# Kernel tuning notes

Measured on AMD Instinct MI355X. Metric: run time of the kernel, lower is better.

Reference implementation:

```python
import jax, jax.numpy as jnp
import numpy as np

# dims (match init_kwargs)
L, D, H, K = 8, 384, 6, 64            # layers, hidden, rwkv heads, rwkv head dim
DI, MH, HD, DS, CK = 768, 12, 64, 64, 4  # mamba: d_inner, heads, head_dim, d_state, conv kernel
V, B, T = 32000, 1, 1024


def _rms(x, w, eps=1e-6):
    return w * x * jax.lax.rsqrt(jnp.mean(x * x, axis=-1, keepdims=True) + eps)


def _rwkv6(xn, Wr, Wk, Wv, Wg, Ww, w_bias, u, gn_w, gn_b, Wo):
    # RWKV6: data-dependent diagonal-decay linear attention
    Bb, Tt, Dd = xn.shape
    proj = lambda W: (xn @ W).reshape(Bb, Tt, H, K)
    r, k, v = proj(Wr), proj(Wk), proj(Wv)
    g = xn @ Wg                                        # [B,T,D]
    w = (xn @ Ww + w_bias).reshape(Bb, Tt, H, K)
    decay = jnp.exp(-jnp.exp(w))                       # in (0,1)

    def step(S, inp):                                  # S: [B,H,K,K] (key x value)
        r_t, k_t, v_t, d_t = inp                       # each [B,H,K]
        kv = k_t[..., :, None] * v_t[..., None, :]     # [B,H,K,K]
        o = jnp.einsum('bhk,bhkv->bhv', r_t, S + u[None, :, :, None] * kv)
        S = d_t[..., None] * S + kv
        return S, o

    tm = lambda a: jnp.moveaxis(a, 1, 0)               # time-major
    S0 = jnp.zeros((Bb, H, K, K), xn.dtype)
    _, o = jax.lax.scan(step, S0, (tm(r), tm(k), tm(v), tm(decay)))
    o = jnp.moveaxis(o, 0, 1)                          # [B,T,H,K]
    # per-head GroupNorm
    mu = jnp.mean(o, -1, keepdims=True)
    var = jnp.var(o, -1, keepdims=True)
    o = (o - mu) * jax.lax.rsqrt(var + 1e-5) * gn_w.reshape(H, K) + gn_b.reshape(H, K)
    o = o.reshape(Bb, Tt, Dd) * jax.nn.silu(g)
    return o @ Wo


def _mamba2(xn, W_in, conv_w, conv_b, dt_bias, A_log, Dp, mn_w, W_out):
    # Mamba2: selective scan with scalar A per head
    Bb, Tt, Dd = xn.shape
    zxbcdt = xn @ W_in                                 # [B,T, 2*DI + 2*DS + MH]
    z = zxbcdt[..., :DI]
    xBC = zxbcdt[..., DI:DI + DI + 2 * DS]
    dt = jax.nn.softplus(zxbcdt[..., -MH:] + dt_bias)  # [B,T,MH]
    # causal depthwise conv1d, kernel CK
    xp = jnp.pad(xBC, ((0, 0), (CK - 1, 0), (0, 0)))
    xBC = sum(xp[:, j:j + Tt, :] * conv_w[:, j] for j in range(CK)) + conv_b
    xBC = jax.nn.silu(xBC)
    xs = xBC[..., :DI].reshape(Bb, Tt, MH, HD)
    Bm = xBC[..., DI:DI + DS]                          # [B,T,DS]
    Cm = xBC[..., DI + DS:]                            # [B,T,DS]
    A = -jnp.exp(A_log)                                # [MH]

    def step(S, inp):                                  # S: [B,MH,HD,DS]
        x_t, B_t, C_t, dt_t = inp                      # [B,MH,HD],[B,DS],[B,DS],[B,MH]
        dA = jnp.exp(dt_t * A)                         # [B,MH]
        S = dA[..., None, None] * S + (dt_t[..., None] * x_t)[..., None] * B_t[:, None, None, :]
        y = jnp.einsum('bhps,bs->bhp', S, C_t) + Dp[None, :, None] * x_t
        return S, y

    tm = lambda a: jnp.moveaxis(a, 1, 0)
    S0 = jnp.zeros((Bb, MH, HD, DS), xn.dtype)
    _, y = jax.lax.scan(step, S0, (tm(xs), tm(Bm), tm(Cm), tm(dt)))
    y = jnp.moveaxis(y, 0, 1).reshape(Bb, Tt, DI)
    y = _rms(y * jax.nn.silu(z), mn_w)                 # gated RMSNorm
    return y @ W_out


def _forward(x, embed, ln_w, Wr, Wk, Wv, Wg, Ww, w_bias, u, gn_w, gn_b, Wo,
             W_in, conv_w, conv_b, dt_bias, A_log, Dp, mn_w, W_out,
             gw, gb, ffn_ln_w, ffn_w1, ffn_w2, ln_out_w):
    h = jnp.take(embed, x, axis=0)                     # [B,T,D]
    for i in range(L):
        xn = _rms(h, ln_w[i])
        o_r = _rwkv6(xn, Wr[i], Wk[i], Wv[i], Wg[i], Ww[i], w_bias[i], u[i], gn_w[i], gn_b[i], Wo[i])
        o_m = _mamba2(xn, W_in[i], conv_w[i], conv_b[i], dt_bias[i], A_log[i], Dp[i], mn_w[i], W_out[i])
        gate = jax.nn.sigmoid(jnp.concatenate([o_r, o_m], -1) @ gw[i] + gb[i])  # [B,T,1]
        h = h + gate * o_r + (1.0 - gate) * o_m
        hn = _rms(h, ffn_ln_w[i])
        h = h + jax.nn.gelu(hn @ ffn_w1[i], approximate=False) @ ffn_w2[i]
    h = _rms(h, ln_out_w)
    return h @ embed.T                                 # tied head -> [B,T,V]


def setup_inputs() -> dict:
    key = jax.random.key(0)
    ks = iter(jax.random.split(key, 32))
    n = lambda shape, s=0.02: jax.random.normal(next(ks), shape, jnp.float32) * s
    d = {}
    d['x'] = jax.random.randint(next(ks), (B, T), 0, V)
    d['embed'] = n((V, D))
    d['ln_w'] = jnp.ones((L, D), jnp.float32)
    d['Wr'] = n((L, D, D)); d['Wk'] = n((L, D, D)); d['Wv'] = n((L, D, D))
    d['Wg'] = n((L, D, D)); d['Ww'] = n((L, D, D))
    d['w_bias'] = n((L, D), 0.5)
    d['u'] = n((L, H, K), 0.5)
    d['gn_w'] = jnp.ones((L, D), jnp.float32)
    d['gn_b'] = jnp.zeros((L, D), jnp.float32)
    d['Wo'] = n((L, D, D))
    d['W_in'] = n((L, D, 2 * DI + 2 * DS + MH))
    d['conv_w'] = n((L, DI + 2 * DS, CK), 0.2)
    d['conv_b'] = jnp.zeros((L, DI + 2 * DS), jnp.float32)
    d['dt_bias'] = jax.random.uniform(next(ks), (L, MH), jnp.float32, -4.0, -1.0)
    d['A_log'] = jnp.log(jax.random.uniform(next(ks), (L, MH), jnp.float32, 1.0, 16.0))
    d['Dp'] = jnp.ones((L, MH), jnp.float32)
    d['mn_w'] = jnp.ones((L, DI), jnp.float32)
    d['W_out'] = n((L, DI, D))
    d['gw'] = n((L, 2 * D, 1), 0.01)
    d['gb'] = jnp.full((L, 1), float(np.log(0.3 / 0.7)), jnp.float32)
    d['ffn_ln_w'] = jnp.ones((L, D), jnp.float32)
    d['ffn_w1'] = n((L, D, 4 * D))
    d['ffn_w2'] = n((L, 4 * D, D))
    d['ln_out_w'] = jnp.ones((D,), jnp.float32)
    return d


def reference(x, embed, ln_w, Wr, Wk, Wv, Wg, Ww, w_bias, u, gn_w, gn_b, Wo,
              W_in, conv_w, conv_b, dt_bias, A_log, Dp, mn_w, W_out,
              gw, gb, ffn_ln_w, ffn_w1, ffn_w2, ln_out_w):
    return _forward(x, embed, ln_w, Wr, Wk, Wv, Wg, Ww, w_bias, u, gn_w, gn_b, Wo,
                    W_in, conv_w, conv_b, dt_bias, A_log, Dp, mn_w, W_out,
                    gw, gb, ffn_ln_w, ffn_w1, ffn_w2, ln_out_w)
```

## Files before the change

kernel.cpp:

```cpp
#include <hip/hip_runtime.h>
#include <math.h>

#define TT 1024
#define DD 384
#define NH 6
#define DI 768
#define MH 12
#define DS 64
#define NL 8
#define XDIM 1676
#define CONVC 896
#define NV 32000
#define PZS 3712
#define G_OFF 1152
#define W_OFF 1536
#define Z_OFF 1920
#define XBC_OFF 2688
#define DT_OFF 3584
#define CHK 32
#define NCH 32

typedef __attribute__((ext_vector_type(8))) short short8;
typedef __attribute__((ext_vector_type(4))) float f32x4;

__device__ __forceinline__ float siluf(float x) { return x / (1.f + expf(-x)); }
__device__ __forceinline__ float sigmoidf_(float x) { return 1.f / (1.f + expf(-x)); }
__device__ __forceinline__ float geluf(float x) {
  return 0.5f * x * (1.f + erff(x * 0.70710678118654752440f));
}
__device__ __forceinline__ unsigned short f2b(float x) {
  union { float f; unsigned int u; } v; v.f = x;
  unsigned int r = v.u + 0x7fffu + ((v.u >> 16) & 1u);
  return (unsigned short)(r >> 16);
}

#define GLDS(gp, lp) __builtin_amdgcn_global_load_lds( \
    (const __attribute__((address_space(1))) void*)(gp), \
    (__attribute__((address_space(3))) void*)(lp), 16, 0, 0)

template<int EPI>
__global__ __launch_bounds__(256) void gemm_bf16(
    const unsigned short* __restrict__ A, const unsigned short* __restrict__ Bt,
    float* __restrict__ C, unsigned short* __restrict__ Cb, int N, int K, int ldC)
{
  __shared__ unsigned short As[4096];
  __shared__ unsigned short Bs[4096];
  int tid = threadIdx.x;
  int wid = tid >> 6, lane = tid & 63;
  int m0 = blockIdx.y * 64, n0 = blockIdx.x * 64;
  int wr = wid >> 1, wc = wid & 1;
  int r0 = tid >> 3, ch = tid & 7;
  int scs = (ch ^ (r0 & 7)) * 8;
  const unsigned short* ga = A  + (size_t)(m0 + r0) * K + scs;
  const unsigned short* gb = Bt + (size_t)(n0 + r0) * K + scs;
  unsigned short* la = As + wid * 512;
  unsigned short* lb = Bs + wid * 512;
  int fr = lane & 15, fc = lane >> 4;
  f32x4 zz = {0.f, 0.f, 0.f, 0.f};
  f32x4 acc[2][2];
  acc[0][0] = zz; acc[0][1] = zz; acc[1][0] = zz; acc[1][1] = zz;

  int kper = K / (int)gridDim.z;
  int ks = blockIdx.z * kper, ke = ks + kper;
  size_t row32 = (size_t)32 * K;
  for (int k0 = ks; k0 < ke; k0 += 64) {
    GLDS(ga + k0, la);
    GLDS(ga + k0 + row32, la + 2048);
    GLDS(gb + k0, lb);
    GLDS(gb + k0 + row32, lb + 2048);
    __syncthreads();
#pragma unroll
    for (int kh = 0; kh < 2; ++kh) {
      short8 af[2], bf[2];
#pragma unroll
      for (int mg = 0; mg < 2; ++mg) {
        int ar = wr * 32 + mg * 16 + fr;
        af[mg] = *reinterpret_cast<const short8*>(&As[ar * 64 + (((kh * 4 + fc) ^ (ar & 7)) * 8)]);
      }
#pragma unroll
      for (int ng = 0; ng < 2; ++ng) {
        int br = wc * 32 + ng * 16 + fr;
        bf[ng] = *reinterpret_cast<const short8*>(&Bs[br * 64 + (((kh * 4 + fc) ^ (br & 7)) * 8)]);
      }
#pragma unroll
      for (int mg = 0; mg < 2; ++mg)
#pragma unroll
        for (int ng = 0; ng < 2; ++ng)
          acc[mg][ng] = __builtin_amdgcn_mfma_f32_16x16x32_bf16(af[mg], bf[ng], acc[mg][ng], 0, 0, 0);
    }
    __syncthreads();
  }
#pragma unroll
  for (int mg = 0; mg < 2; ++mg)
#pragma unroll
    for (int ng = 0; ng < 2; ++ng) {
      int col = n0 + wc * 32 + ng * 16 + fr;
      if (col < N) {
#pragma unroll
        for (int j = 0; j < 4; ++j) {
          int row = m0 + wr * 32 + mg * 16 + fc * 4 + j;
          if (EPI == 1)      Cb[(size_t)row * ldC + col] = f2b(geluf(acc[mg][ng][j]));
          else if (EPI == 3) atomicAdd(&C[(size_t)row * ldC + col], acc[mg][ng][j]);
          else               C[(size_t)row * ldC + col]  = acc[mg][ng][j];
        }
      }
    }
}

__global__ __launch_bounds__(256) void gemm_dual(
    const unsigned short* __restrict__ A0, const unsigned short* __restrict__ B0t,
    float* __restrict__ C0, int K0, int ld0, int nx0, int nb0,
    const unsigned short* __restrict__ A1, const unsigned short* __restrict__ B1t,
    float* __restrict__ C1, int K1, int ld1, int nx1)
{
  __shared__ unsigned short As[4096];
  __shared__ unsigned short Bs[4096];
  int b = blockIdx.x;
  const unsigned short *A, *Bt; float* C; int K, ldC, bx, by;
  if (b < nb0) { A = A0; Bt = B0t; C = C0; K = K0; ldC = ld0; bx = b % nx0; by = b / nx0; }
  else { b -= nb0; A = A1; Bt = B1t; C = C1; K = K1; ldC = ld1; bx = b % nx1; by = b / nx1; }
  int tid = threadIdx.x;
  int wid = tid >> 6, lane = tid & 63;
  int m0 = by * 64, n0 = bx * 64;
  int wr = wid >> 1, wc = wid & 1;
  int r0 = tid >> 3, ch = tid & 7;
  int scs = (ch ^ (r0 & 7)) * 8;
  const unsigned short* ga = A  + (size_t)(m0 + r0) * K + scs;
  const unsigned short* gb = Bt + (size_t)(n0 + r0) * K + scs;
  unsigned short* la = As + wid * 512;
  unsigned short* lb = Bs + wid * 512;
  int fr = lane & 15, fc = lane >> 4;
  f32x4 zz = {0.f, 0.f, 0.f, 0.f};
  f32x4 acc[2][2];
  acc[0][0] = zz; acc[0][1] = zz; acc[1][0] = zz; acc[1][1] = zz;
  size_t row32 = (size_t)32 * K;
  for (int k0 = 0; k0 < K; k0 += 64) {
    GLDS(ga + k0, la);
    GLDS(ga + k0 + row32, la + 2048);
    GLDS(gb + k0, lb);
    GLDS(gb + k0 + row32, lb + 2048);
    __syncthreads();
#pragma unroll
    for (int kh = 0; kh < 2; ++kh) {
      short8 af[2], bf[2];
#pragma unroll
      for (int mg = 0; mg < 2; ++mg) {
        int ar = wr * 32 + mg * 16 + fr;
        af[mg] = *reinterpret_cast<const short8*>(&As[ar * 64 + (((kh * 4 + fc) ^ (ar & 7)) * 8)]);
      }
#pragma unroll
      for (int ng = 0; ng < 2; ++ng) {
        int br = wc * 32 + ng * 16 + fr;
        bf[ng] = *reinterpret_cast<const short8*>(&Bs[br * 64 + (((kh * 4 + fc) ^ (br & 7)) * 8)]);
      }
#pragma unroll
      for (int mg = 0; mg < 2; ++mg)
#pragma unroll
        for (int ng = 0; ng < 2; ++ng)
          acc[mg][ng] = __builtin_amdgcn_mfma_f32_16x16x32_bf16(af[mg], bf[ng], acc[mg][ng], 0, 0, 0);
    }
    __syncthreads();
  }
#pragma unroll
  for (int mg = 0; mg < 2; ++mg)
#pragma unroll
    for (int ng = 0; ng < 2; ++ng) {
      int col = n0 + wc * 32 + ng * 16 + fr;
#pragma unroll
      for (int j = 0; j < 4; ++j) {
        int row = m0 + wr * 32 + mg * 16 + fc * 4 + j;
        C[(size_t)row * ldC + col] = acc[mg][ng][j];
      }
    }
}

__global__ __launch_bounds__(256) void gemm128(
    const unsigned short* __restrict__ A, const unsigned short* __restrict__ Bt,
    float* __restrict__ C, int N, int K, int ldC)
{
  __shared__ unsigned short As[8192];
  __shared__ unsigned short Bs[8192];
  int tid = threadIdx.x;
  int wid = tid >> 6, lane = tid & 63;
  int m0 = blockIdx.y * 128, n0 = blockIdx.x * 128;
  int wr = wid >> 1, wc = wid & 1;
  int r0 = tid >> 3, ch = tid & 7;
  int scs = (ch ^ (r0 & 7)) * 8;
  const unsigned short* ga = A  + (size_t)(m0 + r0) * K + scs;
  const unsigned short* gb = Bt + (size_t)(n0 + r0) * K + scs;
  int fr = lane & 15, fc = lane >> 4;
  f32x4 zz = {0.f, 0.f, 0.f, 0.f};
  f32x4 acc[4][4];
#pragma unroll
  for (int i = 0; i < 4; i++)
#pragma unroll
    for (int j = 0; j < 4; j++) acc[i][j] = zz;

  size_t row32 = (size_t)32 * K;
  for (int k0 = 0; k0 < K; k0 += 64) {
#pragma unroll
    for (int i = 0; i < 4; ++i) {
      GLDS(ga + k0 + i * row32, As + i * 2048 + wid * 512);
      GLDS(gb + k0 + i * row32, Bs + i * 2048 + wid * 512);
    }
    __syncthreads();
#pragma unroll
    for (int kh = 0; kh < 2; ++kh) {
      short8 af[4], bf[4];
#pragma unroll
      for (int mg = 0; mg < 4; ++mg) {
        int ar = wr * 64 + mg * 16 + fr;
        af[mg] = *reinterpret_cast<const short8*>(&As[ar * 64 + (((kh * 4 + fc) ^ (ar & 7)) * 8)]);
      }
#pragma unroll
      for (int ng = 0; ng < 4; ++ng) {
        int br = wc * 64 + ng * 16 + fr;
        bf[ng] = *reinterpret_cast<const short8*>(&Bs[br * 64 + (((kh * 4 + fc) ^ (br & 7)) * 8)]);
      }
#pragma unroll
      for (int mg = 0; mg < 4; ++mg)
#pragma unroll
        for (int ng = 0; ng < 4; ++ng)
          acc[mg][ng] = __builtin_amdgcn_mfma_f32_16x16x32_bf16(af[mg], bf[ng], acc[mg][ng], 0, 0, 0);
    }
    __syncthreads();
  }
#pragma unroll
  for (int mg = 0; mg < 4; ++mg)
#pragma unroll
    for (int ng = 0; ng < 4; ++ng) {
      int col = n0 + wc * 64 + ng * 16 + fr;
      if (col < N) {
#pragma unroll
        for (int j = 0; j < 4; ++j) {
          int row = m0 + wr * 64 + mg * 16 + fc * 4 + j;
          C[(size_t)row * ldC + col] = acc[mg][ng][j];
        }
      }
    }
}

struct TCJob { const float* src; unsigned short* dst; int K, N, Npad, nx; size_t sStr, dStr; int tend; };
struct TC10 { TCJob j[10]; };

__global__ __launch_bounds__(256) void transconv_all(TC10 P)
{
  __shared__ float tile[32][33];
  int bid = blockIdx.x;
  int q = 0;
  while (bid >= P.j[q].tend) ++q;
  int tstart = (q == 0) ? 0 : P.j[q - 1].tend;
  TCJob jb = P.j[q];
  int local = bid - tstart;
  int bx = local % jb.nx, by = local / jb.nx;
  const float* src = jb.src + (size_t)blockIdx.y * jb.sStr;
  unsigned short* dst = jb.dst + (size_t)blockIdx.y * jb.dStr;
  int k0 = by * 32, n0 = bx * 32;
  int tx = threadIdx.x & 31, ty = threadIdx.x >> 5;
  for (int i = ty; i < 32; i += 8) {
    int k = k0 + i, n = n0 + tx;
    tile[i][tx] = (k < jb.K && n < jb.N) ? src[(size_t)k * jb.N + n] : 0.f;
  }
  __syncthreads();
  for (int i = ty; i < 32; i += 8) {
    int n = n0 + i, k = k0 + tx;
    if (n < jb.Npad && k < jb.K) dst[(size_t)n * jb.K + k] = f2b(tile[tx][i]);
  }
}

__global__ void conv_b16_kernel(const float* __restrict__ src, unsigned short* __restrict__ dst, int n)
{
  int idx = blockIdx.x * 256 + threadIdx.x;
  if (idx < n) dst[idx] = f2b(src[idx]);
}

__global__ void embed_kernel(const int* __restrict__ x, const float* __restrict__ embed,
                             float* __restrict__ h)
{
  int idx = blockIdx.x * 256 + threadIdx.x;
  if (idx < TT * DD) {
    int t = idx / DD, d = idx % DD;
    h[idx] = embed[(size_t)x[t] * DD + d];
  }
}

__global__ __launch_bounds__(256) void rms_kernel(const float* __restrict__ in,
                                                  const float* __restrict__ w,
                                                  unsigned short* __restrict__ out)
{
  int row = blockIdx.x * 4 + (threadIdx.x >> 6);
  int lane = threadIdx.x & 63;
  const float* r = in + (size_t)row * DD;
  float v[6]; float ss = 0.f;
#pragma unroll
  for (int j = 0; j < 6; ++j) { v[j] = r[lane + j * 64]; ss = fmaf(v[j], v[j], ss); }
#pragma unroll
  for (int s = 1; s < 64; s <<= 1) ss += __shfl_xor(ss, s);
  float scale = rsqrtf(ss * (1.f / DD) + 1e-6f);
#pragma unroll
  for (int j = 0; j < 6; ++j)
    out[(size_t)row * DD + lane + j * 64] = f2b(w[lane + j * 64] * v[j] * scale);
}

__global__ __launch_bounds__(256) void scanA_kernel(
    const float* __restrict__ PZ, const float* __restrict__ u, const float* __restrict__ wbias,
    float* __restrict__ so, float* __restrict__ rPb,
    float* __restrict__ MstR, float* __restrict__ DcR,
    const float* __restrict__ cw, const float* __restrict__ cbia,
    const float* __restrict__ dtbias,
    const float* __restrict__ Alog, const float* __restrict__ Dpw,
    float* __restrict__ yb, float* __restrict__ Ccb,
    float* __restrict__ MstM, float* __restrict__ DcM)
{
  __shared__ float smem[2 * 256 + 64];
  int b = blockIdx.x, tid = threadIdx.x;
  if (b < 192) {
    int h = b >> 5, c = b & 31;
    float* sbuf = smem; float* us = smem + 512;
    if (tid < 64) us[tid] = u[h * 64 + tid];
    int wv = tid >> 6, l = tid & 63;
    int vv = wv * 16 + (l & 15);
    int kc = l >> 4;
    int arr = tid >> 6, idx = tid & 63;
    int off = (arr == 0) ? 0 : (arr == 1) ? 384 : (arr == 2) ? W_OFF : 768;
    float wb = (arr == 2) ? wbias[h * 64 + idx] : 0.f;
    size_t base = (size_t)h * 64 + idx + off;
    int t0 = c * CHK;
    float S[16], Pc[16];
#pragma unroll
    for (int i = 0; i < 16; i++) { S[i] = 0.f; Pc[i] = 1.f; }
    float reg = PZ[(size_t)t0 * PZS + base];
    bool st = (wv == 0) && ((l & 15) == 0);
    for (int t = 0; t < CHK; ++t) {
      int tt = t0 + t;
      float* cb = sbuf + (t & 1) * 256;
      cb[arr * 64 + idx] = (arr == 2) ? expf(-expf(reg + wb)) : reg;
      if (t + 1 < CHK) reg = PZ[(size_t)(tt + 1) * PZS + base];
      __syncthreads();
      float vt = cb[192 + vv];
      float acc = 0.f;
      float rp[16];
#pragma unroll
      for (int i = 0; i < 16; ++i) {
        int kk = kc * 16 + i;
        float rv = cb[kk], kv = cb[64 + kk], dv = cb[128 + kk];
        rp[i] = rv * Pc[i];
        float kvv = kv * vt;
        acc = fmaf(rv, fmaf(us[kk], kvv, S[i]), acc);
        S[i] = fmaf(dv, S[i], kvv);
        Pc[i] *= dv;
      }
      acc += __shfl_xor(acc, 16);
      acc += __shfl_xor(acc, 32);
      if (l < 16) so[(size_t)tt * DD + h * 64 + vv] = acc;
      if (st) {
        float4* dst = (float4*)&rPb[(size_t)tt * DD + h * 64 + kc * 16];
        dst[0] = make_float4(rp[0], rp[1], rp[2], rp[3]);
        dst[1] = make_float4(rp[4], rp[5], rp[6], rp[7]);
        dst[2] = make_float4(rp[8], rp[9], rp[10], rp[11]);
        dst[3] = make_float4(rp[12], rp[13], rp[14], rp[15]);
      }
    }
    float* ms = MstR + (size_t)(h * NCH + c) * 4096;
    float4* msv = (float4*)&ms[vv * 64 + kc * 16];
    msv[0] = make_float4(S[0], S[1], S[2], S[3]);
    msv[1] = make_float4(S[4], S[5], S[6], S[7]);
    msv[2] = make_float4(S[8], S[9], S[10], S[11]);
    msv[3] = make_float4(S[12], S[13], S[14], S[15]);
    if (st) {
      float4* dd_ = (float4*)&DcR[(h * NCH + c) * 64 + kc * 16];
      dd_[0] = make_float4(Pc[0], Pc[1], Pc[2], Pc[3]);
      dd_[1] = make_float4(Pc[4], Pc[5], Pc[6], Pc[7]);
      dd_[2] = make_float4(Pc[8], Pc[9], Pc[10], Pc[11]);
      dd_[3] = make_float4(Pc[12], Pc[13], Pc[14], Pc[15]);
    }
  } else {
    int bb = b - 192;
    int hh = bb >> 5, c = bb & 31;
    float* sbuf = smem;
    int wv = tid >> 6, l = tid & 63;
    int p = wv * 16 + (l & 15);
    int sc = l >> 4;
    int arr = tid >> 6, idx = tid & 63;
    float A = -expf(Alog[hh]);
    float Dph = Dpw[hh];
    float dtbh = dtbias[hh];
    int t0 = c * CHK;
    float cw0 = 0.f, cw1 = 0.f, cw2 = 0.f, cw3 = 0.f, cbv = 0.f;
    float xw0 = 0.f, xw1 = 0.f, xw2 = 0.f, cur = 0.f;
    const float* xcol = nullptr;
    float reg = 0.f;
    if (arr < 3) {
      int chn = (arr == 0) ? (hh * 64 + idx) : (arr == 1) ? (DI + idx) : (DI + DS + idx);
      cw0 = cw[chn * 4 + 0]; cw1 = cw[chn * 4 + 1]; cw2 = cw[chn * 4 + 2]; cw3 = cw[chn * 4 + 3];
      cbv = cbia[chn];
      xcol = PZ + XBC_OFF + chn;
      xw0 = (t0 >= 3) ? xcol[(size_t)(t0 - 3) * PZS] : 0.f;
      xw1 = (t0 >= 2) ? xcol[(size_t)(t0 - 2) * PZS] : 0.f;
      xw2 = (t0 >= 1) ? xcol[(size_t)(t0 - 1) * PZS] : 0.f;
      cur = xcol[(size_t)t0 * PZS];
    } else {
      reg = PZ[(size_t)t0 * PZS + DT_OFF + hh];
    }
    float S[16]; float cdA = 1.f;
#pragma unroll
    for (int i = 0; i < 16; i++) S[i] = 0.f;
    bool st = (wv == 0) && ((l & 15) == 0);
    for (int t = 0; t < CHK; ++t) {
      int tt = t0 + t;
      float* cb = sbuf + (t & 1) * 256;
      if (arr < 3) {
        float cvv = fmaf(cw3, cur, fmaf(cw2, xw2, fmaf(cw1, xw1, fmaf(cw0, xw0, cbv))));
        cb[arr * 64 + idx] = siluf(cvv);
        float nx = (t + 1 < CHK) ? xcol[(size_t)(tt + 1) * PZS] : 0.f;
        xw0 = xw1; xw1 = xw2; xw2 = cur; cur = nx;
      } else {
        if (idx == 0) {
          float v = reg + dtbh;
          cb[192] = (v > 20.f) ? v : log1pf(expf(v));
        }
        if (t + 1 < CHK) reg = PZ[(size_t)(tt + 1) * PZS + DT_OFF + hh];
      }
      __syncthreads();
      float dt_ = cb[192];
      float dA = expf(dt_ * A);
      cdA *= dA;
      float xp = cb[p];
      float dtx = dt_ * xp;
      float acc = 0.f;
#pragma unroll
      for (int i = 0; i < 16; ++i) {
        int s = sc * 16 + i;
        S[i] = fmaf(dA, S[i], dtx * cb[64 + s]);
        acc = fmaf(S[i], cb[128 + s], acc);
      }
      acc += __shfl_xor(acc, 16);
      acc += __shfl_xor(acc, 32);
      if (l < 16) yb[(size_t)tt * DI + hh * 64 + p] = fmaf(Dph, xp, acc);
      if (st) {
        float4* dst = (float4*)&Ccb[(size_t)tt * DI + hh * 64 + sc * 16];
#pragma unroll
        for (int j4 = 0; j4 < 4; ++j4)
          dst[j4] = make_float4(cdA * cb[128 + sc * 16 + j4 * 4 + 0],
                                cdA * cb[128 + sc * 16 + j4 * 4 + 1],
                                cdA * cb[128 + sc * 16 + j4 * 4 + 2],
                                cdA * cb[128 + sc * 16 + j4 * 4 + 3]);
      }
    }
    float* ms = MstM + (size_t)(hh * NCH + c) * 4096;
    float4* msv = (float4*)&ms[p * 64 + sc * 16];
    msv[0] = make_float4(S[0], S[1], S[2], S[3]);
    msv[1] = make_float4(S[4], S[5], S[6], S[7]);
    msv[2] = make_float4(S[8], S[9], S[10], S[11]);
    msv[3] = make_float4(S[12], S[13], S[14], S[15]);
    if (tid == 0) DcM[hh * NCH + c] = cdA;
  }
}

__global__ __launch_bounds__(256) void corr_kernel(
    const float* __restrict__ MstR, const float* __restrict__ DcR,
    const float* __restrict__ rPb, const float* __restrict__ so,
    const float* __restrict__ MstM, const float* __restrict__ DcM,
    const float* __restrict__ Ccb, float* __restrict__ yb,
    const float* __restrict__ PZ, const float* __restrict__ gnw, const float* __restrict__ gnb,
    unsigned short* __restrict__ gob)
{
  __shared__ float S0l[64 * 68];
  __shared__ float Rl[CHK * 68];
  int b = blockIdx.x, tid = threadIdx.x;
  const float* rg; int ostride, obase, t0;
  bool rwkv = (b < 192);
  int h, cidx;
  if (rwkv) {
    h = b >> 5; cidx = b & 31;
    rg = rPb; obase = h * 64; ostride = DD;
  } else {
    int bb = b - 192; h = bb >> 5; cidx = bb & 31;
    rg = Ccb; obase = h * 64; ostride = DI;
  }
  t0 = cidx * CHK;
  float Sreg[16];
#pragma unroll
  for (int it = 0; it < 16; ++it) Sreg[it] = 0.f;
  if (rwkv) {
    int kk = tid & 63;
    for (int cp = 0; cp < cidx; ++cp) {
      float d = DcR[(h * NCH + cp) * 64 + kk];
      const float* mb = MstR + (size_t)(h * NCH + cp) * 4096;
#pragma unroll
      for (int it = 0; it < 16; ++it)
        Sreg[it] = fmaf(d, Sreg[it], mb[tid + 256 * it]);
    }
  } else {
    for (int cp = 0; cp < cidx; ++cp) {
      float d = DcM[h * NCH + cp];
      const float* mb = MstM + (size_t)(h * NCH + cp) * 4096;
#pragma unroll
      for (int it = 0; it < 16; ++it)
        Sreg[it] = fmaf(d, Sreg[it], mb[tid + 256 * it]);
    }
  }
#pragma unroll
  for (int it = 0; it < 16; ++it) {
    int gi = tid + 256 * it;
    S0l[(gi & 63) * 68 + (gi >> 6)] = Sreg[it];
  }
  {
    int t = tid >> 3, q = (tid & 7) * 8;
    const float4* src = (const float4*)&rg[(size_t)(t0 + t) * ostride + obase + q];
    float4* dst = (float4*)&Rl[t * 68 + q];
    dst[0] = src[0]; dst[1] = src[1];
  }
  __syncthreads();
  int t = tid >> 3, q = (tid & 7) * 8;
  float acc[8];
#pragma unroll
  for (int j = 0; j < 8; j++) acc[j] = 0.f;
  for (int k = 0; k < 64; ++k) {
    float rv = Rl[t * 68 + k];
    const float4* sp = (const float4*)&S0l[k * 68 + q];
    float4 s0 = sp[0], s1 = sp[1];
    acc[0] = fmaf(rv, s0.x, acc[0]);
    acc[1] = fmaf(rv, s0.y, acc[1]);
    acc[2] = fmaf(rv, s0.z, acc[2]);
    acc[3] = fmaf(rv, s0.w, acc[3]);
    acc[4] = fmaf(rv, s1.x, acc[4]);
    acc[5] = fmaf(rv, s1.y, acc[5]);
    acc[6] = fmaf(rv, s1.z, acc[6]);
    acc[7] = fmaf(rv, s1.w, acc[7]);
  }
  if (!rwkv) {
    float4* op = (float4*)&yb[(size_t)(t0 + t) * DI + obase + q];
    float4 c0 = op[0], c1 = op[1];
    c0.x += acc[0]; c0.y += acc[1]; c0.z += acc[2]; c0.w += acc[3];
    c1.x += acc[4]; c1.y += acc[5]; c1.z += acc[6]; c1.w += acc[7];
    op[0] = c0; op[1] = c1;
  } else {
    float ov[8];
    const float4* sp = (const float4*)&so[(size_t)(t0 + t) * DD + obase + q];
    float4 s0 = sp[0], s1 = sp[1];
    ov[0] = s0.x + acc[0]; ov[1] = s0.y + acc[1]; ov[2] = s0.z + acc[2]; ov[3] = s0.w + acc[3];
    ov[4] = s1.x + acc[4]; ov[5] = s1.y + acc[5]; ov[6] = s1.z + acc[6]; ov[7] = s1.w + acc[7];
    float m_ = 0.f;
#pragma unroll
    for (int j = 0; j < 8; j++) m_ += ov[j];
    m_ += __shfl_xor(m_, 1); m_ += __shfl_xor(m_, 2); m_ += __shfl_xor(m_, 4);
    float mu = m_ * (1.f / 64.f);
    float vv = 0.f;
#pragma unroll
    for (int j = 0; j < 8; j++) { float d = ov[j] - mu; vv = fmaf(d, d, vv); }
    vv += __shfl_xor(vv, 1); vv += __shfl_xor(vv, 2); vv += __shfl_xor(vv, 4);
    float rstd = rsqrtf(vv * (1.f / 64.f) + 1e-5f);
#pragma unroll
    for (int j = 0; j < 8; j++) {
      int d = obase + q + j;
      float gv = PZ[(size_t)(t0 + t) * PZS + G_OFF + d];
      float o = fmaf((ov[j] - mu) * rstd, gnw[d], gnb[d]) * siluf(gv);
      gob[(size_t)(t0 + t) * DD + d] = f2b(o);
    }
  }
}

__global__ __launch_bounds__(256) void mamba_norm_kernel(const float* __restrict__ yb,
    const float* __restrict__ PZ, const float* __restrict__ mnw, unsigned short* __restrict__ out)
{
  int row = blockIdx.x * 4 + (threadIdx.x >> 6);
  int lane = threadIdx.x & 63;
  float v[12]; float ss = 0.f;
#pragma unroll
  for (int j = 0; j < 12; ++j) {
    int c = lane + j * 64;
    float z = PZ[(size_t)row * PZS + Z_OFF + c];
    float t = yb[(size_t)row * DI + c] * siluf(z);
    v[j] = t; ss = fmaf(t, t, ss);
  }
#pragma unroll
  for (int s = 1; s < 64; s <<= 1) ss += __shfl_xor(ss, s);
  float scale = rsqrtf(ss * (1.f / DI) + 1e-6f);
#pragma unroll
  for (int j = 0; j < 12; ++j) {
    int c = lane + j * 64;
    out[(size_t)row * DI + c] = f2b(v[j] * scale * mnw[c]);
  }
}

__global__ __launch_bounds__(256) void gate_rms_kernel(const float* __restrict__ orb,
    const float* __restrict__ omb, const float* __restrict__ gw,
    const float* __restrict__ gb, const float* __restrict__ flnw,
    float* __restrict__ h, unsigned short* __restrict__ xnb)
{
  int row = blockIdx.x * 4 + (threadIdx.x >> 6);
  int lane = threadIdx.x & 63;
  float a[6], bq[6]; float ss = 0.f;
#pragma unroll
  for (int j = 0; j < 6; ++j) {
    int c = lane + j * 64;
    a[j] = orb[(size_t)row * DD + c]; bq[j] = omb[(size_t)row * DD + c];
    ss += a[j] * gw[c] + bq[j] * gw[DD + c];
  }
#pragma unroll
  for (int s = 1; s < 64; s <<= 1) ss += __shfl_xor(ss, s);
  float gate = sigmoidf_(ss + gb[0]);
  float hn[6]; float ss2 = 0.f;
#pragma unroll
  for (int j = 0; j < 6; ++j) {
    int c = lane + j * 64;
    size_t ix = (size_t)row * DD + c;
    hn[j] = h[ix] + gate * a[j] + (1.f - gate) * bq[j];
    h[ix] = hn[j];
    ss2 = fmaf(hn[j], hn[j], ss2);
  }
#pragma unroll
  for (int s = 1; s < 64; s <<= 1) ss2 += __shfl_xor(ss2, s);
  float scale = rsqrtf(ss2 * (1.f / DD) + 1e-6f);
#pragma unroll
  for (int j = 0; j < 6; ++j) {
    int c = lane + j * 64;
    xnb[(size_t)row * DD + c] = f2b(flnw[c] * hn[j] * scale);
  }
}

extern "C" void kernel_launch(void* const* d_in, const int* in_sizes, int n_in,
                              void* d_out, int out_size, void* d_ws, size_t ws_size,
                              hipStream_t stream)
{
  const int*   x        = (const int*)  d_in[0];
  const float* embed    = (const float*)d_in[1];
  const float* ln_w     = (const float*)d_in[2];
  const float* Wr       = (const float*)d_in[3];
  const float* Wk       = (const float*)d_in[4];
  const float* Wv       = (const float*)d_in[5];
  const float* Wg       = (const float*)d_in[6];
  const float* Ww       = (const float*)d_in[7];
  const float* w_bias   = (const float*)d_in[8];
  const float* u        = (const float*)d_in[9];
  const float* gn_w     = (const float*)d_in[10];
  const float* gn_b     = (const float*)d_in[11];
  const float* Wo       = (const float*)d_in[12];
  const float* W_in     = (const float*)d_in[13];
  const float* conv_w   = (const float*)d_in[14];
  const float* conv_b   = (const float*)d_in[15];
  const float* dt_bias  = (const float*)d_in[16];
  const float* A_log    = (const float*)d_in[17];
  const float* Dp       = (const float*)d_in[18];
  const float* mn_w     = (const float*)d_in[19];
  const float* W_out    = (const float*)d_in[20];
  const float* gw       = (const float*)d_in[21];
  const float* gb       = (const float*)d_in[22];
  const float* ffn_ln_w = (const float*)d_in[23];
  const float* ffn_w1   = (const float*)d_in[24];
  const float* ffn_w2   = (const float*)d_in[25];
  const float* ln_out_w = (const float*)d_in[26];

  char* base = (char*)d_ws;
  size_t off = 0;
  auto alloc = [&](size_t bytes) { off = (off + 255) & ~(size_t)255; void* p = base + off; off += bytes; return p; };

  float* h    = (float*)alloc((size_t)TT * DD * 4);
  float* PZ   = (float*)alloc((size_t)TT * PZS * 4);
  float* yb   = (float*)alloc((size_t)TT * DI * 4);
  float* so   = (float*)alloc((size_t)TT * DD * 4);
  float* orb  = (float*)alloc((size_t)TT * DD * 4);
  float* omb  = (float*)alloc((size_t)TT * DD * 4);
  float* rPb  = (float*)alloc((size_t)TT * DD * 4);
  float* Ccb  = (float*)alloc((size_t)TT * DI * 4);
  float* MstR = (float*)alloc((size_t)NH * NCH * 4096 * 4);
  float* DcR  = (float*)alloc((size_t)NH * NCH * 64 * 4);
  float* MstM = (float*)alloc((size_t)MH * NCH * 4096 * 4);
  float* DcM  = (float*)alloc((size_t)MH * NCH * 4);
  unsigned short* xnb = (unsigned short*)alloc((size_t)TT * DD * 2);
  unsigned short* gob = (unsigned short*)alloc((size_t)TT * DD * 2);
  unsigned short* ynb = (unsigned short*)alloc((size_t)TT * DI * 2);
  unsigned short* fhb = (unsigned short*)alloc((size_t)TT * 1536 * 2);
  unsigned short* WallT = (unsigned short*)alloc((size_t)NL * PZS * 384 * 2);
  unsigned short* WoT   = (unsigned short*)alloc((size_t)NL * 384 * 384 * 2);
  unsigned short* WoutT = (unsigned short*)alloc((size_t)NL * 384 * 768 * 2);
  unsigned short* F1T   = (unsigned short*)alloc((size_t)NL * 1536 * 384 * 2);
  unsigned short* F2T   = (unsigned short*)alloc((size_t)NL * 384 * 1536 * 2);
  unsigned short* embB  = (unsigned short*)alloc((size_t)NV * DD * 2);
  (void)ws_size; (void)in_sizes; (void)n_in; (void)out_size;

  dim3 blk(256);
  int gTD = (TT * DD + 255) / 256;

  TC10 tc;
  int te = 0;
  auto setjob = [&](int q, const float* src, unsigned short* dst, int K, int N, int Npad,
                    int nx, int ny, size_t sStr, size_t dStr) {
    te += nx * ny;
    tc.j[q] = TCJob{src, dst, K, N, Npad, nx, sStr, dStr, te};
  };
  setjob(0, Wr, WallT + (size_t)0 * 384 * 384, 384, 384, 384, 12, 12, (size_t)384 * 384, (size_t)PZS * 384);
  setjob(1, Wk, WallT + (size_t)1 * 384 * 384, 384, 384, 384, 12, 12, (size_t)384 * 384, (size_t)PZS * 384);
  setjob(2, Wv, WallT + (size_t)2 * 384 * 384, 384, 384, 384, 12, 12, (size_t)384 * 384, (size_t)PZS * 384);
  setjob(3, Wg, WallT + (size_t)3 * 384 * 384, 384, 384, 384, 12, 12, (size_t)384 * 384, (size_t)PZS * 384);
  setjob(4, Ww, WallT + (size_t)4 * 384 * 384, 384, 384, 384, 12, 12, (size_t)384 * 384, (size_t)PZS * 384);
  setjob(5, W_in, WallT + (size_t)1920 * 384, 384, XDIM, 1792, 56, 12, (size_t)384 * XDIM, (size_t)PZS * 384);
  setjob(6, Wo, WoT, 384, 384, 384, 12, 12, (size_t)384 * 384, (size_t)384 * 384);
  setjob(7, W_out, WoutT, 768, 384, 384, 12, 24, (size_t)768 * 384, (size_t)384 * 768);
  setjob(8, ffn_w1, F1T, 384, 1536, 1536, 48, 12, (size_t)384 * 1536, (size_t)1536 * 384);
  setjob(9, ffn_w2, F2T, 1536, 384, 384, 12, 48, (size_t)1536 * 384, (size_t)384 * 1536);
  transconv_all<<<dim3(te, 8), blk, 0, stream>>>(tc);
  conv_b16_kernel<<<(NV * DD + 255) / 256, blk, 0, stream>>>(embed, embB, NV * DD);
  embed_kernel<<<gTD, blk, 0, stream>>>(x, embed, h);

  for (int i = 0; i < NL; ++i) {
    rms_kernel<<<256, blk, 0, stream>>>(h, ln_w + (size_t)i * DD, xnb);

    gemm_bf16<0><<<dim3(58, 16), blk, 0, stream>>>(
        xnb, WallT + (size_t)i * PZS * 384, PZ, nullptr, PZS, 384, PZS);

    scanA_kernel<<<576, blk, 0, stream>>>(PZ, u + (size_t)i * NH * 64, w_bias + (size_t)i * DD,
                                          so, rPb, MstR, DcR,
                                          conv_w + (size_t)i * CONVC * 4, conv_b + (size_t)i * CONVC,
                                          dt_bias + (size_t)i * MH,
                                          A_log + (size_t)i * MH, Dp + (size_t)i * MH,
                                          yb, Ccb, MstM, DcM);
    corr_kernel<<<576, blk, 0, stream>>>(MstR, DcR, rPb, so, MstM, DcM, Ccb, yb,
                                         PZ, gn_w + (size_t)i * DD, gn_b + (size_t)i * DD, gob);

    mamba_norm_kernel<<<256, blk, 0, stream>>>(yb, PZ, mn_w + (size_t)i * DI, ynb);

    gemm_dual<<<192, blk, 0, stream>>>(
        gob, WoT + (size_t)i * 384 * 384, orb, 384, DD, 6, 96,
        ynb, WoutT + (size_t)i * 384 * 768, omb, 768, DD, 6);

    gate_rms_kernel<<<256, blk, 0, stream>>>(orb, omb, gw + (size_t)i * 2 * DD, gb + i,
                                             ffn_ln_w + (size_t)i * DD, h, xnb);

    gemm_bf16<1><<<dim3(24, 16), blk, 0, stream>>>(
        xnb, F1T + (size_t)i * 1536 * 384, nullptr, fhb, 1536, 384, 1536);
    gemm_bf16<3><<<dim3(6, 16, 4), blk, 0, stream>>>(
        fhb, F2T + (size_t)i * 384 * 1536, h, nullptr, DD, 1536, DD);
  }

  rms_kernel<<<256, blk, 0, stream>>>(h, ln_out_w, xnb);
  gemm128<<<dim3(250, 8), blk, 0, stream>>>(
      xnb, embB, (float*)d_out, NV, 384, NV);
}
```

Baseline: 983.0 us.

## Remap LM-head GEMM tiles per XCD and stage stores through LDS

The final vocabulary GEMM now uses a 1D grid whose block index is remapped so that consecutive blocks on each XCD share the same embedding column tiles, which is meant to improve L2 reuse of the B operand. The epilogue stages each warp's accumulator fragment in shared memory and writes full rows with float4 stores, giving coalesced writes of the large fp32 logits output. The col<N guard is dropped, which holds only because 32000 is a multiple of 128. The staging adds extra syncthreads per tile.

```diff
diff --git a/kernel.cpp b/kernel.cpp
--- a/kernel.cpp
+++ b/kernel.cpp
@@ -178,11 +178,15 @@
     const unsigned short* __restrict__ A, const unsigned short* __restrict__ Bt,
     float* __restrict__ C, int N, int K, int ldC)
 {
-  __shared__ unsigned short As[8192];
-  __shared__ unsigned short Bs[8192];
+  __shared__ __align__(16) char smraw[32768];
+  unsigned short* As = (unsigned short*)smraw;
+  unsigned short* Bs = (unsigned short*)smraw + 8192;
   int tid = threadIdx.x;
   int wid = tid >> 6, lane = tid & 63;
-  int m0 = blockIdx.y * 128, n0 = blockIdx.x * 128;
+  int bb = blockIdx.x;
+  int xcd = bb & 7, ii = bb >> 3;
+  int tt = xcd * 250 + ii;
+  int m0 = (tt & 7) * 128, n0 = (tt >> 3) * 128;
   int wr = wid >> 1, wc = wid & 1;
   int r0 = tid >> 3, ch = tid & 7;
   int scs = (ch ^ (r0 & 7)) * 8;
@@ -225,19 +229,23 @@
     }
     __syncthreads();
   }
-#pragma unroll
-  for (int mg = 0; mg < 4; ++mg)
-#pragma unroll
-    for (int ng = 0; ng < 4; ++ng) {
-      int col = n0 + wc * 64 + ng * 16 + fr;
-      if (col < N) {
-#pragma unroll
-        for (int j = 0; j < 4; ++j) {
-          int row = m0 + wr * 64 + mg * 16 + fc * 4 + j;
-          C[(size_t)row * ldC + col] = acc[mg][ng][j];
-        }
-      }
-    }
+  float* wst = (float*)smraw + wid * 1088;
+  int rr = lane >> 2, q = (lane & 3) * 16;
+#pragma unroll
+  for (int mg = 0; mg < 4; ++mg) {
+#pragma unroll
+    for (int ng = 0; ng < 4; ++ng)
+#pragma unroll
+      for (int j = 0; j < 4; ++j)
+        wst[(fc * 4 + j) * 68 + ng * 16 + fr] = acc[mg][ng][j];
+    __syncthreads();
+    int row = m0 + wr * 64 + mg * 16 + rr;
+    size_t rb = (size_t)row * ldC + n0 + wc * 64 + q;
+#pragma unroll
+    for (int i = 0; i < 4; ++i)
+      *(float4*)&C[rb + i * 4] = *(const float4*)&wst[rr * 68 + q + i * 4];
+    __syncthreads();
+  }
 }
 
 struct TCJob { const float* src; unsigned short* dst; int K, N, Npad, nx; size_t sStr, dStr; int tend; };
@@ -731,10 +739,10 @@
     gemm_bf16<1><<<dim3(24, 16), blk, 0, stream>>>(
         xnb, F1T + (size_t)i * 1536 * 384, nullptr, fhb, 1536, 384, 1536);
     gemm_bf16<3><<<dim3(6, 16, 4), blk, 0, stream>>>(
-        fhb, F2T + (size_t)i * 384 * 1536, h, nullptr, DD, 1536, DD);
+        fhb, F2T + (size_t)i * 384 * 1536, h, nullptr, 384, 1536, 384);
   }
 
   rms_kernel<<<256, blk, 0, stream>>>(h, ln_out_w, xnb);
-  gemm128<<<dim3(250, 8), blk, 0, stream>>>(
+  gemm128<<<dim3(2000), blk, 0, stream>>>(
       xnb, embB, (float*)d_out, NV, 384, NV);
 }
```

Measured after the change: 993.0 us (median of 2 runs). About the same (+1.0%).
